# Kernel tuning notes

Hardware: AMD Instinct MI355X
Metric: run time of the kernel (lower is better)

## Reference

```python
import jax, jax.numpy as jnp
import numpy as np

TEMPERATURE = 1.0

def setup_inputs() -> dict:
    key = jax.random.key(0)
    k1, k2, k3 = jax.random.split(key, 3)
    B, N, D = 1024, 256, 512
    return {
        "fg_img_feature": jax.random.normal(k1, (B, D), dtype=jnp.float32),
        "fg_pro_feature": jax.random.normal(k2, (B, D), dtype=jnp.float32),
        "bg_pro_feature": jax.random.normal(k3, (B, N, D), dtype=jnp.float32),
    }

def reference(fg_img_feature, fg_pro_feature, bg_pro_feature):
    # Only the image features are L2-normalized (matches original module).
    img = fg_img_feature / jnp.linalg.norm(fg_img_feature, axis=-1, keepdims=True)  # [B, D]
    # Per-sample scalar logit: img_i . fg_pro_i
    pos_logits = jnp.sum(img * fg_pro_feature, axis=-1) / TEMPERATURE  # [B]
    # Per-sample batched matvec against N background prototypes.
    bg_logits = jnp.einsum('bd,bnd->bn', img, bg_pro_feature) / TEMPERATURE  # [B, N]
    positive_sims = jnp.sum(jnp.exp(pos_logits))
    negative_sims = positive_sims + jnp.sum(jnp.exp(bg_logits))
    return -jnp.log(positive_sims / negative_sims)
```

## Files before the change

### kernel.cpp

```cpp
#include <hip/hip_runtime.h>
#include <hip/hip_bf16.h>
#include <math.h>


#define D_DIM   512
#define NSPLIT  2

__global__ __launch_bounds__(256) void infonce_main(
    const float* __restrict__ img,
    const float* __restrict__ fg_pro,
    const float* __restrict__ bg_pro,
    float* __restrict__ accum,
    int N)
{
    const int b     = blockIdx.x >> 1;
    const int split = blockIdx.x & 1;
    const int tid   = threadIdx.x;
    const int wid   = tid >> 6;
    const int lane  = tid & 63;

    __shared__ float s_img[D_DIM];
    __shared__ float s_red[8];

    const float2 v = reinterpret_cast<const float2*>(img + (size_t)b * D_DIM)[tid];
    float ss = v.x * v.x + v.y * v.y;
    #pragma unroll
    for (int off = 32; off > 0; off >>= 1) ss += __shfl_xor(ss, off);
    if (lane == 0) s_red[wid] = ss;
    __syncthreads();
    const float inv = rsqrtf(s_red[0] + s_red[1] + s_red[2] + s_red[3]);

    const float2 nv = make_float2(v.x * inv, v.y * inv);
    reinterpret_cast<float2*>(s_img)[tid] = nv;

    if (split == 0) {
        const float2 p = reinterpret_cast<const float2*>(fg_pro + (size_t)b * D_DIM)[tid];
        float pd = nv.x * p.x + nv.y * p.y;
        #pragma unroll
        for (int off = 32; off > 0; off >>= 1) pd += __shfl_xor(pd, off);
        if (lane == 0) s_red[4 + wid] = pd;
    }
    __syncthreads();
    if (split == 0 && tid == 0) {
        const float pos = s_red[4] + s_red[5] + s_red[6] + s_red[7];
        atomicAdd(&accum[0], expf(pos));
    }

    const int rows_per_block = N / NSPLIT;
    const int rows_per_wave  = rows_per_block / 4;
    const int n0 = split * rows_per_block + wid * rows_per_wave;

    const float4* s_img4 = reinterpret_cast<const float4*>(s_img);
    const float4  a0 = s_img4[lane];
    const float4  a1 = s_img4[64 + lane];

    const float4* bg4 = reinterpret_cast<const float4*>(bg_pro + (size_t)b * N * D_DIM);
    float local = 0.0f;

    for (int i = 0; i < rows_per_wave; i += 4) {
        const float4* r0 = bg4 + (size_t)(n0 + i + 0) * (D_DIM / 4);
        const float4* r1 = bg4 + (size_t)(n0 + i + 1) * (D_DIM / 4);
        const float4* r2 = bg4 + (size_t)(n0 + i + 2) * (D_DIM / 4);
        const float4* r3 = bg4 + (size_t)(n0 + i + 3) * (D_DIM / 4);
        const float4 b00 = r0[lane], b01 = r0[64 + lane];
        const float4 b10 = r1[lane], b11 = r1[64 + lane];
        const float4 b20 = r2[lane], b21 = r2[64 + lane];
        const float4 b30 = r3[lane], b31 = r3[64 + lane];

        float d0 = a0.x*b00.x + a0.y*b00.y + a0.z*b00.z + a0.w*b00.w
                 + a1.x*b01.x + a1.y*b01.y + a1.z*b01.z + a1.w*b01.w;
        float d1 = a0.x*b10.x + a0.y*b10.y + a0.z*b10.z + a0.w*b10.w
                 + a1.x*b11.x + a1.y*b11.y + a1.z*b11.z + a1.w*b11.w;
        float d2 = a0.x*b20.x + a0.y*b20.y + a0.z*b20.z + a0.w*b20.w
                 + a1.x*b21.x + a1.y*b21.y + a1.z*b21.z + a1.w*b21.w;
        float d3 = a0.x*b30.x + a0.y*b30.y + a0.z*b30.z + a0.w*b30.w
                 + a1.x*b31.x + a1.y*b31.y + a1.z*b31.z + a1.w*b31.w;

        #pragma unroll
        for (int off = 32; off > 0; off >>= 1) {
            d0 += __shfl_xor(d0, off);
            d1 += __shfl_xor(d1, off);
            d2 += __shfl_xor(d2, off);
            d3 += __shfl_xor(d3, off);
        }
        if (lane == 0)
            local += expf(d0) + expf(d1) + expf(d2) + expf(d3);
    }

    if (lane == 0) s_red[wid] = local;
    __syncthreads();
    if (tid == 0)
        atomicAdd(&accum[1], s_red[0] + s_red[1] + s_red[2] + s_red[3]);
}

__global__ void infonce_finalize(const float* __restrict__ accum,
                                 float* __restrict__ out)
{
    const float pos = accum[0];
    const float neg = accum[1];
    out[0] = logf(pos + neg) - logf(pos);
}

extern "C" void kernel_launch(void* const* d_in, const int* in_sizes, int n_in,
                              void* d_out, int out_size, void* d_ws, size_t ws_size,
                              hipStream_t stream)
{
    const float* img = (const float*)d_in[0];
    const float* fg  = (const float*)d_in[1];
    const float* bg  = (const float*)d_in[2];
    float* out   = (float*)d_out;
    float* accum = (float*)d_ws;

    const int B = in_sizes[0] / D_DIM;
    const int N = in_sizes[2] / in_sizes[0];

    hipMemsetAsync(accum, 0, 2 * sizeof(float), stream);
    infonce_main<<<B * NSPLIT, 256, 0, stream>>>(img, fg, bg, accum, N);
    infonce_finalize<<<1, 1, 0, stream>>>(accum, out);
}
```

Before: 679.4 us.

## Split each sample across four blocks and fully unroll row loads before reductions

Doubles the per-sample block split to four so each wave handles a fixed 16 rows, and fully unrolls the row loop so all row loads and partial dot products are issued before any cross-lane shuffle reduction. The goal is more memory-level parallelism and more blocks in flight for this bandwidth-bound matvec. In exchange, register pressure rises, the image normalisation is recomputed by more blocks, and the code now hardcodes N equal to 256 through the fixed rows-per-wave constant.

```diff
diff --git a/kernel.cpp b/kernel.cpp
--- a/kernel.cpp
+++ b/kernel.cpp
@@ -4,7 +4,8 @@
 
 
 #define D_DIM   512
-#define NSPLIT  2
+#define NSPLIT  4
+#define ROWS_PER_WAVE 16
 
 __global__ __launch_bounds__(256) void infonce_main(
     const float* __restrict__ img,
@@ -13,8 +14,8 @@
     float* __restrict__ accum,
     int N)
 {
-    const int b     = blockIdx.x >> 1;
-    const int split = blockIdx.x & 1;
+    const int b     = blockIdx.x >> 2;
+    const int split = blockIdx.x & 3;
     const int tid   = threadIdx.x;
     const int wid   = tid >> 6;
     const int lane  = tid & 63;
@@ -46,36 +47,43 @@
         atomicAdd(&accum[0], expf(pos));
     }
 
-    const int rows_per_block = N / NSPLIT;
-    const int rows_per_wave  = rows_per_block / 4;
-    const int n0 = split * rows_per_block + wid * rows_per_wave;
+    const int n0 = split * (N / NSPLIT) + wid * ROWS_PER_WAVE;
 
     const float4* s_img4 = reinterpret_cast<const float4*>(s_img);
     const float4  a0 = s_img4[lane];
     const float4  a1 = s_img4[64 + lane];
 
-    const float4* bg4 = reinterpret_cast<const float4*>(bg_pro + (size_t)b * N * D_DIM);
-    float local = 0.0f;
+    const float4* bg4 = reinterpret_cast<const float4*>(
+        bg_pro + (size_t)b * N * D_DIM + (size_t)n0 * D_DIM);
 
-    for (int i = 0; i < rows_per_wave; i += 4) {
-        const float4* r0 = bg4 + (size_t)(n0 + i + 0) * (D_DIM / 4);
-        const float4* r1 = bg4 + (size_t)(n0 + i + 1) * (D_DIM / 4);
-        const float4* r2 = bg4 + (size_t)(n0 + i + 2) * (D_DIM / 4);
-        const float4* r3 = bg4 + (size_t)(n0 + i + 3) * (D_DIM / 4);
+    float part[ROWS_PER_WAVE];
+
+    #pragma unroll
+    for (int i = 0; i < ROWS_PER_WAVE; i += 4) {
+        const float4* r0 = bg4 + (size_t)(i + 0) * (D_DIM / 4);
+        const float4* r1 = bg4 + (size_t)(i + 1) * (D_DIM / 4);
+        const float4* r2 = bg4 + (size_t)(i + 2) * (D_DIM / 4);
+        const float4* r3 = bg4 + (size_t)(i + 3) * (D_DIM / 4);
         const float4 b00 = r0[lane], b01 = r0[64 + lane];
         const float4 b10 = r1[lane], b11 = r1[64 + lane];
         const float4 b20 = r2[lane], b21 = r2[64 + lane];
         const float4 b30 = r3[lane], b31 = r3[64 + lane];
 
-        float d0 = a0.x*b00.x + a0.y*b00.y + a0.z*b00.z + a0.w*b00.w
-                 + a1.x*b01.x + a1.y*b01.y + a1.z*b01.z + a1.w*b01.w;
-        float d1 = a0.x*b10.x + a0.y*b10.y + a0.z*b10.z + a0.w*b10.w
-                 + a1.x*b11.x + a1.y*b11.y + a1.z*b11.z + a1.w*b11.w;
-        float d2 = a0.x*b20.x + a0.y*b20.y + a0.z*b20.z + a0.w*b20.w
-                 + a1.x*b21.x + a1.y*b21.y + a1.z*b21.z + a1.w*b21.w;
-        float d3 = a0.x*b30.x + a0.y*b30.y + a0.z*b30.z + a0.w*b30.w
-                 + a1.x*b31.x + a1.y*b31.y + a1.z*b31.z + a1.w*b31.w;
+        part[i + 0] = a0.x*b00.x + a0.y*b00.y + a0.z*b00.z + a0.w*b00.w
+                    + a1.x*b01.x + a1.y*b01.y + a1.z*b01.z + a1.w*b01.w;
+        part[i + 1] = a0.x*b10.x + a0.y*b10.y + a0.z*b10.z + a0.w*b10.w
+                    + a1.x*b11.x + a1.y*b11.y + a1.z*b11.z + a1.w*b11.w;
+        part[i + 2] = a0.x*b20.x + a0.y*b20.y + a0.z*b20.z + a0.w*b20.w
+                    + a1.x*b21.x + a1.y*b21.y + a1.z*b21.z + a1.w*b21.w;
+        part[i + 3] = a0.x*b30.x + a0.y*b30.y + a0.z*b30.z + a0.w*b30.w
+                    + a1.x*b31.x + a1.y*b31.y + a1.z*b31.z + a1.w*b31.w;
+    }
 
+    float local = 0.0f;
+    #pragma unroll
+    for (int i = 0; i < ROWS_PER_WAVE; i += 4) {
+        float d0 = part[i + 0], d1 = part[i + 1],
+              d2 = part[i + 2], d3 = part[i + 3];
         #pragma unroll
         for (int off = 32; off > 0; off >>= 1) {
             d0 += __shfl_xor(d0, off);
```

Result: no change. 677.6 us (-0.3%).
